# Optimization experiments

Hardware: AMD Instinct MI355X
Metric: run time of the kernel (lower is better)

Reference implementation:

```python
import jax, jax.numpy as jnp
import numpy as np

NEG = -9.0e15


def setup_inputs() -> dict:
    key = jax.random.key(0)
    k_x, k_w, k_e, k_b, k_m = jax.random.split(key, 5)
    B, N, C, F = 2048, 64, 256, 256
    x = jax.random.normal(k_x, (B, N, C), dtype=jnp.float32)
    W = jax.random.normal(k_w, (2, C, F), dtype=jnp.float32) * (1.414 / np.sqrt(C + F))
    # full logit tensor; only entries where mask holds are ever read (equivalent
    # to torch's flat `e` scattered into the nonzero positions of adj)
    e = jax.random.normal(k_e, (F, N, N), dtype=jnp.float32)
    bias = jax.random.normal(k_b, (F,), dtype=jnp.float32) * (1.0 / np.sqrt(C))
    # symmetric adjacency mask with self-loops, density ~0.3
    m = jax.random.bernoulli(k_m, 0.3, (N, N))
    mask = (m | m.T) | jnp.eye(N, dtype=bool)
    return {"x": x, "W": W, "e": e, "bias": bias, "mask": mask}


def reference(x, W, e, bias, mask):
    # x: [B,N,C], W: [2,C,F], e: [F,N,N], bias: [F], mask: [N,N] bool
    h0 = x @ W[0]                                   # [B,N,F] (self term)
    h1 = x @ W[1]                                   # [B,N,F] (neighbor term)
    logits = jnp.where(mask[None, :, :], e, NEG)    # [F,N,N]
    adj = jax.nn.softmax(logits, axis=2)            # per-channel row softmax
    N = mask.shape[0]
    eye = jnp.eye(N, dtype=bool)
    d = jnp.diagonal(adj, axis1=1, axis2=2)         # [F,N]  (adj * E diagonal)
    off = jnp.where(eye[None, :, :], 0.0, adj)      # [F,N,N] (adj * (1-E))
    # (adj*E) @ h0 reduces to per-node diagonal scaling; off-diag is a
    # per-channel NxN matmul batched over B.
    out = d.T[None, :, :] * h0 + jnp.einsum('fnm,bmf->bnf', off, h1)
    return out + bias[None, None, :]
```

## Files before the change

### kernel.cpp

```cpp
#include <hip/hip_runtime.h>
#include <hip/hip_bf16.h>


typedef __attribute__((ext_vector_type(8))) short  fragA;
typedef __attribute__((ext_vector_type(4))) float  f32x4;
typedef __attribute__((ext_vector_type(8))) unsigned short u16x8;
typedef __attribute__((ext_vector_type(4))) unsigned short u16x4;

constexpr long OFF_OFF = 0;
constexpr long OFF_WT  = 2l * 1024 * 1024;
constexpr long OFF_DS  = OFF_WT + 512l * 256 * 2;
constexpr long OFF_XB  = OFF_DS + 64l * 256 * 4;
constexpr long OFF_G0  = OFF_XB + 131072l * 256 * 2;
constexpr long OFF_H1T = OFF_G0 + 131072l * 256 * 2;
constexpr long WS_NEED = OFF_H1T + 131072l * 256 * 2;

static __device__ inline unsigned short f2bf(float f) {
  __hip_bfloat16 h = __float2bfloat16(f);
  return __builtin_bit_cast(unsigned short, h);
}
static __device__ inline float bf2f(unsigned short u) {
  unsigned int x = ((unsigned int)u) << 16;
  return __builtin_bit_cast(float, x);
}
static __device__ __forceinline__ void gl16(const void* g, void* l) {
  __builtin_amdgcn_global_load_lds(
      (const __attribute__((address_space(1))) unsigned int*)g,
      (__attribute__((address_space(3))) unsigned int*)l, 16, 0, 0);
}
static __device__ __forceinline__ f32x4 mfma16(fragA a, fragA b, f32x4 c) {
  return __builtin_amdgcn_mfma_f32_16x16x32_bf16(a, b, c, 0, 0, 0);
}

__global__ __launch_bounds__(256) void k_pre(const float* __restrict__ x,
                                             const float* __restrict__ e,
                                             const float* __restrict__ W,
                                             const unsigned char* __restrict__ mask,
                                             char* __restrict__ ws_b) {
  const int bid = blockIdx.x;
  const int tid = threadIdx.x;
  if (bid < 4096) {
    unsigned short* off = (unsigned short*)(ws_b + OFF_OFF);
    float* dscale = (float*)(ws_b + OFF_DS);
    const int lane = tid & 63;
    const int row  = bid * 4 + (tid >> 6);
    const int n = row & 63;
    bool is_u8 = __all(mask[lane * 65] != 0);
    bool mv;
    if (is_u8) mv = mask[n * 64 + lane] != 0;
    else       mv = ((const int*)mask)[n * 64 + lane] != 0;
    float v = mv ? e[(long)row * 64 + lane] : -1e30f;
    float mx = v;
#pragma unroll
    for (int s = 32; s; s >>= 1) mx = fmaxf(mx, __shfl_xor(mx, s));
    float ex = mv ? __expf(v - mx) : 0.f;
    float sm = ex;
#pragma unroll
    for (int s = 32; s; s >>= 1) sm += __shfl_xor(sm, s);
    float adj = ex / sm;
    const int f = row >> 6;
    if (lane == n) dscale[n * 256 + f] = adj;
    off[(long)row * 64 + lane] = f2bf(lane == n ? 0.f : adj);
  } else if (bid < 6144) {
    unsigned short* xb = (unsigned short*)(ws_b + OFF_XB);
    long i = ((long)(bid - 4096) * 256 + tid) * 8;
    const long stride = 2048l * 256 * 8;
    const long total = 131072l * 256;
    for (; i < total; i += stride) {
      float4 a = *(const float4*)(x + i);
      float4 b = *(const float4*)(x + i + 4);
      u16x8 p;
      p[0] = f2bf(a.x); p[1] = f2bf(a.y); p[2] = f2bf(a.z); p[3] = f2bf(a.w);
      p[4] = f2bf(b.x); p[5] = f2bf(b.y); p[6] = f2bf(b.z); p[7] = f2bf(b.w);
      *(u16x8*)(xb + i) = p;
    }
  } else {
    unsigned short* Wt = (unsigned short*)(ws_b + OFF_WT);
    __shared__ float t[64][65];
    const int b2 = bid - 6144;
    const int w = b2 >> 4, f0 = ((b2 >> 2) & 3) * 64, c0 = (b2 & 3) * 64;
    const int tr = tid >> 2, tc = (tid & 3) * 16;
    const float* src = W + ((long)(w * 256 + c0 + tr)) * 256 + f0 + tc;
#pragma unroll
    for (int i = 0; i < 16; i += 4) {
      float4 v = *(const float4*)(src + i);
      t[tr][tc + i] = v.x; t[tr][tc + i + 1] = v.y;
      t[tr][tc + i + 2] = v.z; t[tr][tc + i + 3] = v.w;
    }
    __syncthreads();
    u16x8 p0, p1;
#pragma unroll
    for (int i = 0; i < 8; i++)  p0[i] = f2bf(t[tc + i][tr]);
#pragma unroll
    for (int i = 0; i < 8; i++)  p1[i] = f2bf(t[tc + 8 + i][tr]);
    unsigned short* dst = Wt + ((long)(w * 256 + f0 + tr)) * 256 + c0 + tc;
    *(u16x8*)dst = p0;
    *(u16x8*)(dst + 8) = p1;
  }
}

__global__ __launch_bounds__(256) void k_gemm(char* __restrict__ ws_b) {
  const float* dscale = (const float*)(ws_b + OFF_DS);
  const char* xb_b = ws_b + OFF_XB;
  const char* wt_b = ws_b + OFF_WT;
  unsigned short* g0g = (unsigned short*)(ws_b + OFF_G0);
  unsigned short* h1t = (unsigned short*)(ws_b + OFF_H1T);

  __shared__ __align__(16) char arena[49152];

  const int tid = threadIdx.x;
  const int wid = tid >> 6, lane = tid & 63;
  const int lr = lane & 15, qu = lane >> 4;

  const int wg = blockIdx.x;
  const int xcd = wg & 7, s = wg >> 3;
  const int rg = xcd * 128 + (s >> 3);
  const int cg = s & 7;
  const int f0 = cg * 32;
  const long R0 = (long)rg * 128;

  const int ar   = tid >> 3;
  const int swz  = (((tid & 7) ^ (ar & 7)) << 4);

  const int bc0 = tid >> 3;
  const int wrow0 = f0 + bc0;
  const int wrow1 = 224 + f0 + (bc0 + 32);

#pragma unroll
  for (int i = 0; i < 4; i++)
    gl16(xb_b + (R0 + i * 32 + ar) * 512 + swz, arena + i * 4096 + tid * 16);
  gl16(wt_b + (long)wrow0 * 512 + swz, arena + 32768 + tid * 16);
  gl16(wt_b + (long)wrow1 * 512 + swz, arena + 32768 + 4096 + tid * 16);

  f32x4 acc[2][4] = {};
  const int arow0 = wid * 32;

  for (int ks = 0; ks < 4; ks++) {
    __syncthreads();
    if (ks < 3) {
      const int nb = (ks + 1) & 1;
      const long ko = (ks + 1) * 128;
#pragma unroll
      for (int i = 0; i < 4; i++)
        gl16(xb_b + (R0 + i * 32 + ar) * 512 + ko + swz,
             arena + nb * 16384 + i * 4096 + tid * 16);
      gl16(wt_b + (long)wrow0 * 512 + ko + swz,
           arena + 32768 + nb * 8192 + tid * 16);
      gl16(wt_b + (long)wrow1 * 512 + ko + swz,
           arena + 32768 + nb * 8192 + 4096 + tid * 16);
    }
    const char* ab = arena + (ks & 1) * 16384;
    const char* bb = arena + 32768 + (ks & 1) * 8192;
    fragA af[2][2], bfr[2][4];
#pragma unroll
    for (int kk = 0; kk < 2; kk++) {
#pragma unroll
      for (int i2 = 0; i2 < 2; i2++) {
        int r = arow0 + i2 * 16 + lr;
        af[kk][i2] = *(const fragA*)(ab + r * 128 +
                        ((kk * 64 + qu * 16) ^ ((lr & 7) << 4)));
      }
#pragma unroll
      for (int j = 0; j < 4; j++) {
        int cc = j * 16 + lr;
        bfr[kk][j] = *(const fragA*)(bb + cc * 128 +
                        ((kk * 64 + qu * 16) ^ ((lr & 7) << 4)));
      }
    }
#pragma unroll
    for (int kk = 0; kk < 2; kk++)
#pragma unroll
      for (int i2 = 0; i2 < 2; i2++)
#pragma unroll
        for (int j = 0; j < 4; j++)
          acc[i2][j] = mfma16(af[kk][i2], bfr[kk][j], acc[i2][j]);
  }
  __syncthreads();

  unsigned short* Gs = (unsigned short*)(arena);
  unsigned short* Ts = (unsigned short*)(arena + 16384);
#pragma unroll
  for (int i2 = 0; i2 < 2; i2++) {
#pragma unroll
    for (int j = 0; j < 2; j++) {
      int f = f0 + j * 16 + lr;
#pragma unroll
      for (int r = 0; r < 4; r++) {
        int rloc = arow0 + i2 * 16 + qu * 4 + r;
        int n = rloc & 63;
        Gs[rloc * 40 + j * 16 + lr] = f2bf(dscale[n * 256 + f] * acc[i2][j][r]);
      }
    }
#pragma unroll
    for (int j = 2; j < 4; j++) {
      int fl = (j - 2) * 16 + lr;
      int rb = arow0 + i2 * 16 + qu * 4;
      u16x4 pk;
      pk[0] = f2bf(acc[i2][j][0]); pk[1] = f2bf(acc[i2][j][1]);
      pk[2] = f2bf(acc[i2][j][2]); pk[3] = f2bf(acc[i2][j][3]);
      *(u16x4*)(Ts + fl * 136 + rb) = pk;
    }
  }
  __syncthreads();

  {
    int row = tid >> 1, half = tid & 1;
    const unsigned short* sp = Gs + row * 40 + half * 16;
    unsigned short* dp = g0g + (R0 + row) * 256 + f0 + half * 16;
    *(u16x8*)dp = *(const u16x8*)sp;
    *(u16x8*)(dp + 8) = *(const u16x8*)(sp + 8);
  }
  {
    int f = tid >> 3, seg = tid & 7;
    const unsigned short* sp = Ts + f * 136 + seg * 16;
    unsigned short* dp = h1t + (long)(f0 + f) * 131072 + R0 + seg * 16;
    *(u16x8*)dp = *(const u16x8*)sp;
    *(u16x8*)(dp + 8) = *(const u16x8*)(sp + 8);
  }
}

__global__ __launch_bounds__(256) void k_eout(const float* __restrict__ bias,
                                              const char* __restrict__ ws_b,
                                              float* __restrict__ out) {
  const unsigned short* offp = (const unsigned short*)(ws_b + OFF_OFF);
  const unsigned short* h1t  = (const unsigned short*)(ws_b + OFF_H1T);
  const unsigned short* g0g  = (const unsigned short*)(ws_b + OFF_G0);

  __shared__ __align__(16) unsigned short Es[16 * 64 * 18];

  const int tid = threadIdx.x;
  const int wid = tid >> 6, lane = tid & 63;
  const int lr = lane & 15, qu = lane >> 4;

  const int wg = blockIdx.x;
  const int xcd = wg & 7, u = wg >> 3;
  const int bg = xcd * 16 + (u >> 4);
  const int fg = u & 15;
  const long B0 = (long)bg * 16;
  const int f0 = fg * 16;

#pragma unroll
  for (int q = 0; q < 4; q++) {
    const int fi = wid * 4 + q;
    const long fglob = f0 + fi;
    const unsigned short* hb_p = h1t + fglob * 131072 + (B0 + lr) * 64;
    const unsigned short* ob   = offp + fglob * 4096;
    fragA hb0 = *(const fragA*)(hb_p + qu * 8);
    fragA hb1 = *(const fragA*)(hb_p + 32 + qu * 8);
    f32x4 ea[4] = {};
#pragma unroll
    for (int ct = 0; ct < 4; ct++) {
      fragA o0 = *(const fragA*)(ob + (ct * 16 + lr) * 64 + qu * 8);
      fragA o1 = *(const fragA*)(ob + (ct * 16 + lr) * 64 + 32 + qu * 8);
      ea[ct] = mfma16(o0, hb0, ea[ct]);
      ea[ct] = mfma16(o1, hb1, ea[ct]);
    }
    const int fsw = fi ^ ((lr & 3) << 2);
#pragma unroll
    for (int ct = 0; ct < 4; ct++)
#pragma unroll
      for (int r = 0; r < 4; r++) {
        int n = ct * 16 + qu * 4 + r;
        Es[lr * 1152 + n * 18 + fsw] = f2bf(ea[ct][r]);
      }
  }
  __syncthreads();

  float4 bv[4];
#pragma unroll
  for (int k = 0; k < 4; k++) bv[k] = ((const float4*)(bias + f0))[k];
#pragma unroll
  for (int i = 0; i < 4; i++) {
    int rl = tid + 256 * i;
    int b = rl >> 6, n = rl & 63;
    long gRow = (B0 + b) * 64 + n;
    const unsigned short* gp = g0g + gRow * 256 + f0;
    u16x8 gv0 = ((const u16x8*)gp)[0];
    u16x8 gv1 = ((const u16x8*)gp)[1];
    u16x4 ev[4];
#pragma unroll
    for (int gg = 0; gg < 4; gg++)
      ev[gg] = *(const u16x4*)&Es[b * 1152 + n * 18 + ((gg << 2) ^ ((b & 3) << 2))];
    float4* op = (float4*)(out + gRow * 256 + f0);
#pragma unroll
    for (int k = 0; k < 4; k++) {
      float4 ov;
      float g0e = bf2f(k < 2 ? gv0[(k & 1) * 4 + 0] : gv1[(k & 1) * 4 + 0]);
      float g1e = bf2f(k < 2 ? gv0[(k & 1) * 4 + 1] : gv1[(k & 1) * 4 + 1]);
      float g2e = bf2f(k < 2 ? gv0[(k & 1) * 4 + 2] : gv1[(k & 1) * 4 + 2]);
      float g3e = bf2f(k < 2 ? gv0[(k & 1) * 4 + 3] : gv1[(k & 1) * 4 + 3]);
      ov.x = g0e + bf2f(ev[k][0]) + bv[k].x;
      ov.y = g1e + bf2f(ev[k][1]) + bv[k].y;
      ov.z = g2e + bf2f(ev[k][2]) + bv[k].z;
      ov.w = g3e + bf2f(ev[k][3]) + bv[k].w;
      op[k] = ov;
    }
  }
}

extern "C" void kernel_launch(void* const* d_in, const int* in_sizes, int n_in,
                              void* d_out, int out_size, void* d_ws, size_t ws_size,
                              hipStream_t stream) {
  const float* x    = (const float*)d_in[0];
  const float* W    = (const float*)d_in[1];
  const float* e    = (const float*)d_in[2];
  const float* bias = (const float*)d_in[3];
  const unsigned char* mask = (const unsigned char*)d_in[4];
  float* out = (float*)d_out;
  char* ws = (char*)d_ws;
  if (ws_size < (size_t)WS_NEED) return;

  k_pre<<<6176, 256, 0, stream>>>(x, e, W, mask, ws);
  k_gemm<<<8192, 256, 0, stream>>>(ws);
  k_eout<<<2048, 256, 0, stream>>>(bias, ws, out);
}
```

Measured before the change: 227.0 us.

## Single-buffer GEMM LDS for occupancy and restructure eout prefetch and LDS layout

k_gemm drops LDS double buffering (48KB to 24KB) and adds a launch bound of 5 waves per SIMD, so more workgroups fit per CU. The cost is that the next k-slice load no longer overlaps the MFMAs. k_eout hoists the h1t fragment loads and the g0/bias loads ahead of the MFMA and LDS phases to hide latency, and switches the Es LDS layout to f-major with packed 4-wide stores and scalar strided reads. This raises register pressure under the new launch bounds.

```diff
diff --git a/kernel.cpp b/kernel.cpp
--- a/kernel.cpp
+++ b/kernel.cpp
@@ -99,14 +99,14 @@
   }
 }
 
-__global__ __launch_bounds__(256) void k_gemm(char* __restrict__ ws_b) {
+__global__ __launch_bounds__(256, 5) void k_gemm(char* __restrict__ ws_b) {
   const float* dscale = (const float*)(ws_b + OFF_DS);
   const char* xb_b = ws_b + OFF_XB;
   const char* wt_b = ws_b + OFF_WT;
   unsigned short* g0g = (unsigned short*)(ws_b + OFF_G0);
   unsigned short* h1t = (unsigned short*)(ws_b + OFF_H1T);
 
-  __shared__ __align__(16) char arena[49152];
+  __shared__ __align__(16) char arena[24576];
 
   const int tid = threadIdx.x;
   const int wid = tid >> 6, lane = tid & 63;
@@ -120,65 +120,53 @@
   const long R0 = (long)rg * 128;
 
   const int ar   = tid >> 3;
-  const int swz  = (((tid & 7) ^ (ar & 7)) << 4);
-
-  const int bc0 = tid >> 3;
-  const int wrow0 = f0 + bc0;
-  const int wrow1 = 224 + f0 + (bc0 + 32);
-
-#pragma unroll
-  for (int i = 0; i < 4; i++)
-    gl16(xb_b + (R0 + i * 32 + ar) * 512 + swz, arena + i * 4096 + tid * 16);
-  gl16(wt_b + (long)wrow0 * 512 + swz, arena + 32768 + tid * 16);
-  gl16(wt_b + (long)wrow1 * 512 + swz, arena + 32768 + 4096 + tid * 16);
-
+  const int aswz = (((tid & 7) ^ (ar & 7)) << 4);
+  const int wrow0 = f0 + ar;
+  const int wrow1 = 256 + f0 + ar;
+
+  auto STAGE = [&](int ks) {
+    const long ko = (long)ks * 128;
+#pragma unroll
+    for (int i = 0; i < 4; i++)
+      gl16(xb_b + (R0 + i * 32 + ar) * 512 + ko + aswz,
+           arena + i * 4096 + tid * 16);
+    gl16(wt_b + (long)wrow0 * 512 + ko + aswz, arena + 16384 + tid * 16);
+    gl16(wt_b + (long)wrow1 * 512 + ko + aswz, arena + 16384 + 4096 + tid * 16);
+  };
+
+  STAGE(0);
   f32x4 acc[2][4] = {};
   const int arow0 = wid * 32;
 
   for (int ks = 0; ks < 4; ks++) {
     __syncthreads();
-    if (ks < 3) {
-      const int nb = (ks + 1) & 1;
-      const long ko = (ks + 1) * 128;
-#pragma unroll
-      for (int i = 0; i < 4; i++)
-        gl16(xb_b + (R0 + i * 32 + ar) * 512 + ko + swz,
-             arena + nb * 16384 + i * 4096 + tid * 16);
-      gl16(wt_b + (long)wrow0 * 512 + ko + swz,
-           arena + 32768 + nb * 8192 + tid * 16);
-      gl16(wt_b + (long)wrow1 * 512 + ko + swz,
-           arena + 32768 + nb * 8192 + 4096 + tid * 16);
-    }
-    const char* ab = arena + (ks & 1) * 16384;
-    const char* bb = arena + 32768 + (ks & 1) * 8192;
-    fragA af[2][2], bfr[2][4];
 #pragma unroll
     for (int kk = 0; kk < 2; kk++) {
+      fragA af[2], bfr[4];
 #pragma unroll
       for (int i2 = 0; i2 < 2; i2++) {
         int r = arow0 + i2 * 16 + lr;
-        af[kk][i2] = *(const fragA*)(ab + r * 128 +
-                        ((kk * 64 + qu * 16) ^ ((lr & 7) << 4)));
+        af[i2] = *(const fragA*)(arena + r * 128 +
+                     ((kk * 64 + qu * 16) ^ ((lr & 7) << 4)));
       }
 #pragma unroll
       for (int j = 0; j < 4; j++) {
         int cc = j * 16 + lr;
-        bfr[kk][j] = *(const fragA*)(bb + cc * 128 +
-                        ((kk * 64 + qu * 16) ^ ((lr & 7) << 4)));
+        bfr[j] = *(const fragA*)(arena + 16384 + cc * 128 +
+                     ((kk * 64 + qu * 16) ^ ((lr & 7) << 4)));
       }
-    }
-#pragma unroll
-    for (int kk = 0; kk < 2; kk++)
 #pragma unroll
       for (int i2 = 0; i2 < 2; i2++)
 #pragma unroll
         for (int j = 0; j < 4; j++)
-          acc[i2][j] = mfma16(af[kk][i2], bfr[kk][j], acc[i2][j]);
-  }
-  __syncthreads();
+          acc[i2][j] = mfma16(af[i2], bfr[j], acc[i2][j]);
+    }
+    __syncthreads();
+    if (ks < 3) STAGE(ks + 1);
+  }
 
   unsigned short* Gs = (unsigned short*)(arena);
-  unsigned short* Ts = (unsigned short*)(arena + 16384);
+  unsigned short* Ts = (unsigned short*)(arena + 10240);
 #pragma unroll
   for (int i2 = 0; i2 < 2; i2++) {
 #pragma unroll
@@ -219,14 +207,14 @@
   }
 }
 
-__global__ __launch_bounds__(256) void k_eout(const float* __restrict__ bias,
-                                              const char* __restrict__ ws_b,
-                                              float* __restrict__ out) {
+__global__ __launch_bounds__(256, 4) void k_eout(const float* __restrict__ bias,
+                                                 const char* __restrict__ ws_b,
+                                                 float* __restrict__ out) {
   const unsigned short* offp = (const unsigned short*)(ws_b + OFF_OFF);
   const unsigned short* h1t  = (const unsigned short*)(ws_b + OFF_H1T);
   const unsigned short* g0g  = (const unsigned short*)(ws_b + OFF_G0);
 
-  __shared__ __align__(16) unsigned short Es[16 * 64 * 18];
+  __shared__ __align__(16) unsigned short Es[16 * 1088];
 
   const int tid = threadIdx.x;
   const int wid = tid >> 6, lane = tid & 63;
@@ -239,60 +227,67 @@
   const long B0 = (long)bg * 16;
   const int f0 = fg * 16;
 
+  fragA hb0[4], hb1[4];
+#pragma unroll
+  for (int q = 0; q < 4; q++) {
+    const unsigned short* hp =
+        h1t + (long)(f0 + wid * 4 + q) * 131072 + (B0 + lr) * 64 + qu * 8;
+    hb0[q] = *(const fragA*)hp;
+    hb1[q] = *(const fragA*)(hp + 32);
+  }
+
 #pragma unroll
   for (int q = 0; q < 4; q++) {
     const int fi = wid * 4 + q;
-    const long fglob = f0 + fi;
-    const unsigned short* hb_p = h1t + fglob * 131072 + (B0 + lr) * 64;
-    const unsigned short* ob   = offp + fglob * 4096;
-    fragA hb0 = *(const fragA*)(hb_p + qu * 8);
-    fragA hb1 = *(const fragA*)(hb_p + 32 + qu * 8);
+    const unsigned short* ob = offp + (long)(f0 + fi) * 4096;
     f32x4 ea[4] = {};
 #pragma unroll
     for (int ct = 0; ct < 4; ct++) {
       fragA o0 = *(const fragA*)(ob + (ct * 16 + lr) * 64 + qu * 8);
       fragA o1 = *(const fragA*)(ob + (ct * 16 + lr) * 64 + 32 + qu * 8);
-      ea[ct] = mfma16(o0, hb0, ea[ct]);
-      ea[ct] = mfma16(o1, hb1, ea[ct]);
-    }
-    const int fsw = fi ^ ((lr & 3) << 2);
-#pragma unroll
-    for (int ct = 0; ct < 4; ct++)
-#pragma unroll
-      for (int r = 0; r < 4; r++) {
-        int n = ct * 16 + qu * 4 + r;
-        Es[lr * 1152 + n * 18 + fsw] = f2bf(ea[ct][r]);
-      }
-  }
-  __syncthreads();
-
-  float4 bv[4];
-#pragma unroll
-  for (int k = 0; k < 4; k++) bv[k] = ((const float4*)(bias + f0))[k];
+      ea[ct] = mfma16(o0, hb0[q], ea[ct]);
+      ea[ct] = mfma16(o1, hb1[q], ea[ct]);
+    }
+#pragma unroll
+    for (int ct = 0; ct < 4; ct++) {
+      u16x4 pk;
+      pk[0] = f2bf(ea[ct][0]); pk[1] = f2bf(ea[ct][1]);
+      pk[2] = f2bf(ea[ct][2]); pk[3] = f2bf(ea[ct][3]);
+      *(u16x4*)&Es[fi * 1088 + lr * 68 + ct * 16 + qu * 4] = pk;
+    }
+  }
+
+  u16x8 gv[4][2];
 #pragma unroll
   for (int i = 0; i < 4; i++) {
     int rl = tid + 256 * i;
     int b = rl >> 6, n = rl & 63;
-    long gRow = (B0 + b) * 64 + n;
-    const unsigned short* gp = g0g + gRow * 256 + f0;
-    u16x8 gv0 = ((const u16x8*)gp)[0];
-    u16x8 gv1 = ((const u16x8*)gp)[1];
-    u16x4 ev[4];
-#pragma unroll
-    for (int gg = 0; gg < 4; gg++)
-      ev[gg] = *(const u16x4*)&Es[b * 1152 + n * 18 + ((gg << 2) ^ ((b & 3) << 2))];
-    float4* op = (float4*)(out + gRow * 256 + f0);
+    const unsigned short* gp = g0g + ((B0 + b) * 64 + n) * 256 + f0;
+    gv[i][0] = ((const u16x8*)gp)[0];
+    gv[i][1] = ((const u16x8*)gp)[1];
+  }
+  float4 bv[4];
+#pragma unroll
+  for (int k = 0; k < 4; k++) bv[k] = ((const float4*)(bias + f0))[k];
+
+  __syncthreads();
+
+#pragma unroll
+  for (int i = 0; i < 4; i++) {
+    int rl = tid + 256 * i;
+    int b = rl >> 6, n = rl & 63;
+    float es[16];
+#pragma unroll
+    for (int k = 0; k < 16; k++)
+      es[k] = bf2f(Es[k * 1088 + b * 68 + n]);
+    float4* op = (float4*)(out + ((B0 + b) * 64 + n) * 256 + f0);
 #pragma unroll
     for (int k = 0; k < 4; k++) {
       float4 ov;
-      float g0e = bf2f(k < 2 ? gv0[(k & 1) * 4 + 0] : gv1[(k & 1) * 4 + 0]);
-      float g1e = bf2f(k < 2 ? gv0[(k & 1) * 4 + 1] : gv1[(k & 1) * 4 + 1]);
-      float g2e = bf2f(k < 2 ? gv0[(k & 1) * 4 + 2] : gv1[(k & 1) * 4 + 2]);
-      float g3e = bf2f(k < 2 ? gv0[(k & 1) * 4 + 3] : gv1[(k & 1) * 4 + 3]);
-      ov.x = g0e + bf2f(ev[k][0]) + bv[k].x;
-      ov.y = g1e + bf2f(ev[k][1]) + bv[k].y;
-      ov.z = g2e + bf2f(ev[k][2]) + bv[k].z;
-      ov.w = g3e + bf2f(ev[k][3]) + bv[k].w;
+      ov.x = bf2f(gv[i][k >> 1][(k & 1) * 4 + 0]) + es[k * 4 + 0] + bv[k].x;
+      ov.y = bf2f(gv[i][k >> 1][(k & 1) * 4 + 1]) + es[k * 4 + 1] + bv[k].y;
+      ov.z = bf2f(gv[i][k >> 1][(k & 1) * 4 + 2]) + es[k * 4 + 2] + bv[k].z;
+      ov.w = bf2f(gv[i][k >> 1][(k & 1) * 4 + 3]) + es[k * 4 + 3] + bv[k].w;
       op[k] = ov;
     }
   }
```

New measurement: 216.7 us. -4.6%, faster.
